# Kernel optimization log

Measured on AMD Instinct MI355X. Metric: run time of the kernel, lower is better.

## Reference

```python
import jax, jax.numpy as jnp
import numpy as np

K = 3      # deformable kernel size
PAD = 1    # padding for all 3x3 convs


def conv2d(x, w, b):
    y = jax.lax.conv_general_dilated(x, w, (1, 1), ((PAD, PAD), (PAD, PAD)),
                                     dimension_numbers=('NCHW', 'OIHW', 'NCHW'))
    return y + b[None, :, None, None]


def ln_channels(x, w, b, eps=1e-5):
    # Restormer 'WithBias' LayerNorm: normalize over channel dim of NCHW
    mu = jnp.mean(x, axis=1, keepdims=True)
    var = jnp.mean((x - mu) ** 2, axis=1, keepdims=True)
    return (x - mu) / jnp.sqrt(var + eps) * w[None, :, None, None] + b[None, :, None, None]


def deform_conv(x, offset, mask, weight, bias):
    # x: [B,Cin,H,W], offset: [B,2*K*K,H,W] (dy,dx interleaved), mask: [B,K*K,H,W]
    B, Cin, H, W = x.shape
    Kk = K * K
    off = offset.reshape(B, Kk, 2, H, W)
    dy, dx = off[:, :, 0], off[:, :, 1]                     # [B,Kk,H,W]
    ky, kx = jnp.meshgrid(jnp.arange(K), jnp.arange(K), indexing='ij')
    ky = (ky.reshape(-1) - PAD).astype(x.dtype)             # [Kk]
    kx = (kx.reshape(-1) - PAD).astype(x.dtype)
    py = jnp.arange(H, dtype=x.dtype)[None, None, :, None] + ky[None, :, None, None] + dy
    px = jnp.arange(W, dtype=x.dtype)[None, None, None, :] + kx[None, :, None, None] + dx
    y0 = jnp.floor(py); x0 = jnp.floor(px)
    wy1 = py - y0; wx1 = px - x0
    xf = x.reshape(B, Cin, H * W)

    def corner(yc, xc, wgt):
        valid = (yc >= 0) & (yc <= H - 1) & (xc >= 0) & (xc <= W - 1)
        yi = jnp.clip(yc, 0, H - 1).astype(jnp.int32)
        xi = jnp.clip(xc, 0, W - 1).astype(jnp.int32)
        idx = (yi * W + xi).reshape(B, -1)                  # [B, Kk*H*W]
        v = jax.vmap(lambda xb, ib: xb[:, ib])(xf, idx)     # [B, Cin, Kk*H*W]
        v = v.reshape(B, Cin, Kk, H, W)
        return v * (wgt * valid.astype(x.dtype))[:, None]

    sampled = (corner(y0, x0, (1 - wy1) * (1 - wx1))
               + corner(y0, x0 + 1, (1 - wy1) * wx1)
               + corner(y0 + 1, x0, wy1 * (1 - wx1))
               + corner(y0 + 1, x0 + 1, wy1 * wx1))         # [B,Cin,Kk,H,W]
    sampled = sampled * mask[:, None]                        # modulated (DCNv2)
    wk = weight.reshape(weight.shape[0], Cin, Kk)            # [Cout,Cin,Kk]
    out = jnp.einsum('bckhw,ock->bohw', sampled, wk)
    return out + bias[None, :, None, None]


def setup_inputs() -> dict:
    key = jax.random.key(0)
    ks = jax.random.split(key, 12)
    B, Ce, Cf, H, W = 4, 32, 64, 128, 128
    Cin, Kk = Ce + Cf, K * K
    d = {
        'f_evt_rec': jax.random.normal(ks[0], (B, Ce, H, W), jnp.float32),
        'f_efnet':   jax.random.normal(ks[1], (B, Cf, H, W), jnp.float32),
        'ln_evt_w': jnp.ones((Ce,), jnp.float32), 'ln_evt_b': jnp.zeros((Ce,), jnp.float32),
        'ln_ef_w':  jnp.ones((Cf,), jnp.float32), 'ln_ef_b':  jnp.zeros((Cf,), jnp.float32),
        'ln_al_w':  jnp.ones((Cf,), jnp.float32), 'ln_al_b':  jnp.zeros((Cf,), jnp.float32),
        'off_w': jax.random.normal(ks[2], (2 * Kk, Cin, K, K), jnp.float32) * 0.01,
        'off_b': jnp.zeros((2 * Kk,), jnp.float32),
        'mod_w': jax.random.normal(ks[3], (Kk, Cin, K, K), jnp.float32) * 0.01,
        'mod_b': jnp.zeros((Kk,), jnp.float32),
        'reg_w': jax.random.normal(ks[4], (Cf, Cin, K, K), jnp.float32) * 0.05,
        'reg_b': jnp.zeros((Cf,), jnp.float32),
        'stage_idx': 0,
    }
    return d


def reference(f_evt_rec, f_efnet, ln_evt_w, ln_evt_b, ln_ef_w, ln_ef_b,
              ln_al_w, ln_al_b, off_w, off_b, mod_w, mod_b, reg_w, reg_b, stage_idx):
    e = ln_channels(f_evt_rec, ln_evt_w, ln_evt_b)
    fe = ln_channels(f_efnet, ln_ef_w, ln_ef_b)
    ox = jnp.concatenate([e, fe], axis=1)                    # [B,96,H,W]
    offset = conv2d(ox, off_w, off_b)
    mask = 2.0 * jax.nn.sigmoid(conv2d(ox, mod_w, mod_b))
    al = deform_conv(ox, offset, mask, reg_w, reg_b)         # [B,64,H,W]
    al = jnp.where(al >= 0, al, 0.2 * al)                    # LeakyReLU(0.2)
    al = ln_channels(al, ln_al_w, ln_al_b)
    return al
```

## Files before the change

kernel.cpp:

```cpp
#include <hip/hip_runtime.h>
#include <hip/hip_bf16.h>

#define BATCH 4
#define HH 128
#define WW 128
#define CE 32
#define CF 64
#define CIN 96
#define KK 9
#define COUT 64

typedef __bf16 bf16x8 __attribute__((ext_vector_type(8)));
typedef float f32x4 __attribute__((ext_vector_type(4)));
#define MFMA16(a, b, c) __builtin_amdgcn_mfma_f32_16x16x32_bf16(a, b, c, 0, 0, 0)
typedef union { uint4 u; bf16x8 v; } U8;

#define OX_BYTES   (BATCH * HH * WW * CIN * 2)
#define WCT_OFFB   OX_BYTES
#define WCT_BYTES  (32 * 864 * 2)
#define WKT_OFFB   (WCT_OFFB + WCT_BYTES)

__global__ __launch_bounds__(256) void ln_concat_prep(
    const float* __restrict__ evt, const float* __restrict__ efn,
    const float* __restrict__ w_e, const float* __restrict__ b_e,
    const float* __restrict__ w_f, const float* __restrict__ b_f,
    const float* __restrict__ off_w, const float* __restrict__ mod_w,
    const float* __restrict__ reg_w,
    __hip_bfloat16* __restrict__ ox,
    __hip_bfloat16* __restrict__ wcombT,
    __hip_bfloat16* __restrict__ wkT) {
  __shared__ float vals[64 * 97];
  __shared__ float part[4 * 64 * 4];
  __shared__ float stat[64 * 4];

  {
    int e = blockIdx.x * 256 + threadIdx.x;
    const int TOT1 = 32 * 864, TOT2 = 64 * 864;
    if (e < TOT1) {
      int oc = e / 864, k = e % 864;
      int tap = k / 96, c = k % 96;
      float v = 0.f;
      if (oc < 18)      v = off_w[(oc * CIN + c) * KK + tap];
      else if (oc < 27) v = mod_w[((oc - 18) * CIN + c) * KK + tap];
      wcombT[e] = __float2bfloat16(v);
    } else if (e < TOT1 + TOT2) {
      int e2 = e - TOT1;
      int oc = e2 / 864, k = e2 % 864;
      int tap = k / 96, c = k % 96;
      wkT[e2] = __float2bfloat16(reg_w[(oc * CIN + c) * KK + tap]);
    }
  }

  int bid = blockIdx.x;
  int wg = (bid & 7) * 128 + (bid >> 3);
  int p0 = wg * 64;
  int b = p0 >> 14, y = (p0 >> 7) & 127, x0 = p0 & 127;
  int t = threadIdx.x, px = t & 63, g = t >> 6;

  float sE = 0.f, sE2 = 0.f, sF = 0.f, sF2 = 0.f;
  const float* pe = evt + (((size_t)b * CE) << 14) + (y << 7) + x0 + px;
#pragma unroll
  for (int j = 0; j < 8; ++j) {
    int c = g * 8 + j;
    float v = pe[(size_t)c << 14];
    vals[px * 97 + c] = v; sE += v; sE2 += v * v;
  }
  const float* pf = efn + (((size_t)b * CF) << 14) + (y << 7) + x0 + px;
#pragma unroll
  for (int j = 0; j < 16; ++j) {
    int c = g * 16 + j;
    float v = pf[(size_t)c << 14];
    vals[px * 97 + CE + c] = v; sF += v; sF2 += v * v;
  }
  {
    float4 p4 = {sE, sE2, sF, sF2};
    *(float4*)&part[(g * 64 + px) * 4] = p4;
  }
  __syncthreads();
  if (g == 0) {
    float aE = 0.f, aE2 = 0.f, aF = 0.f, aF2 = 0.f;
#pragma unroll
    for (int gg = 0; gg < 4; ++gg) {
      float4 p4 = *(const float4*)&part[(gg * 64 + px) * 4];
      aE += p4.x; aE2 += p4.y; aF += p4.z; aF2 += p4.w;
    }
    float muE = aE * (1.f / CE);
    float vE = aE2 * (1.f / CE) - muE * muE;
    float muF = aF * (1.f / CF);
    float vF = aF2 * (1.f / CF) - muF * muF;
    float4 s4 = {muE, rsqrtf(vE + 1e-5f), muF, rsqrtf(vF + 1e-5f)};
    *(float4*)&stat[px * 4] = s4;
  }
  __syncthreads();
  uint* orow = (uint*)(ox + (size_t)p0 * CIN);
#pragma unroll
  for (int i = 0; i < 12; ++i) {
    int e = i * 256 + t;
    int xx = e / 48, c = (e % 48) * 2;
    float v0 = vals[xx * 97 + c], v1 = vals[xx * 97 + c + 1];
    float mu, rs, lw0, lb0, lw1, lb1;
    if (c < CE) {
      mu = stat[xx * 4 + 0]; rs = stat[xx * 4 + 1];
      lw0 = w_e[c]; lb0 = b_e[c]; lw1 = w_e[c + 1]; lb1 = b_e[c + 1];
    } else {
      mu = stat[xx * 4 + 2]; rs = stat[xx * 4 + 3];
      lw0 = w_f[c - CE]; lb0 = b_f[c - CE]; lw1 = w_f[c + 1 - CE]; lb1 = b_f[c + 1 - CE];
    }
    float o0 = (v0 - mu) * rs * lw0 + lb0;
    float o1 = (v1 - mu) * rs * lw1 + lb1;
    __hip_bfloat16 h0 = __float2bfloat16(o0), h1 = __float2bfloat16(o1);
    orow[e] = ((uint)*(unsigned short*)&h1 << 16) | (uint)*(unsigned short*)&h0;
  }
}

__device__ __forceinline__ uint blend1(uint u0, uint u1, uint u2, uint u3,
                                       float w0, float w1, float w2, float w3) {
  float lo = w0 * __uint_as_float(u0 << 16) + w1 * __uint_as_float(u1 << 16)
           + w2 * __uint_as_float(u2 << 16) + w3 * __uint_as_float(u3 << 16);
  float hi = w0 * __uint_as_float(u0 & 0xffff0000u) + w1 * __uint_as_float(u1 & 0xffff0000u)
           + w2 * __uint_as_float(u2 & 0xffff0000u) + w3 * __uint_as_float(u3 & 0xffff0000u);
  __hip_bfloat16 bl = __float2bfloat16(lo), bh = __float2bfloat16(hi);
  return ((uint)*(unsigned short*)&bh << 16) | (uint)*(unsigned short*)&bl;
}

__global__ __launch_bounds__(256, 4) void conv_deform_fused(
    const __hip_bfloat16* __restrict__ ox,
    const __hip_bfloat16* __restrict__ wcombT,
    const __hip_bfloat16* __restrict__ wkT,
    const float* __restrict__ off_b, const float* __restrict__ mod_b,
    const float* __restrict__ reg_b,
    const float* __restrict__ lnw, const float* __restrict__ lnb,
    float* __restrict__ out) {
  __shared__ float offm[64 * 28];
  __shared__ float outl[64 * 65];

  int bid = blockIdx.x;
  int wg = (bid & 7) * 128 + (bid >> 3);
  int p0 = wg * 64;
  int b = p0 >> 14, y = (p0 >> 7) & 127, x0 = p0 & 127;
  const __hip_bfloat16* oxb = ox + (((size_t)b) << 14) * CIN;

  int t = threadIdx.x, lane = t & 63, wv = t >> 6;
  int lr = lane & 15, lg = lane >> 4;
  int pxw = (wv << 4) + lr;

  f32x4 cc0 = {0.f,0.f,0.f,0.f}, cc1 = {0.f,0.f,0.f,0.f};
  {
    const __hip_bfloat16* br0 = wcombT + (size_t)lr * 864 + lg * 8;
    const __hip_bfloat16* br1 = wcombT + (size_t)(16 + lr) * 864 + lg * 8;
    for (int tap = 0; tap < 9; ++tap) {
      int yy = y + tap / 3 - 1;
      int xx = x0 + pxw + tap % 3 - 1;
      bool valid = ((unsigned)yy < 128u) && ((unsigned)xx < 128u);
      int cy = min(max(yy, 0), 127), cx = min(max(xx, 0), 127);
      const __hip_bfloat16* arow = oxb + (size_t)((cy << 7) + cx) * CIN + lg * 8;
#pragma unroll
      for (int ks = 0; ks < 3; ++ks) {
        U8 a, w0, w1;
        a.u = *(const uint4*)(arow + ks * 32);
        if (!valid) { a.u.x = 0; a.u.y = 0; a.u.z = 0; a.u.w = 0; }
        w0.u = *(const uint4*)(br0 + tap * 96 + ks * 32);
        w1.u = *(const uint4*)(br1 + tap * 96 + ks * 32);
        cc0 = MFMA16(a.v, w0.v, cc0);
        cc1 = MFMA16(a.v, w1.v, cc1);
      }
    }
  }
#pragma unroll
  for (int nt = 0; nt < 2; ++nt) {
    int oc = nt * 16 + lr;
    if (oc < 27) {
      float bia = (oc < 18) ? off_b[oc] : mod_b[oc - 18];
      f32x4 a = nt ? cc1 : cc0;
#pragma unroll
      for (int r = 0; r < 4; ++r) {
        int pxc = (wv << 4) + (lg << 2) + r;
        float v = a[r] + bia;
        if (oc >= 18) v = 2.f / (1.f + __expf(-v));
        offm[pxc * 28 + oc] = v;
      }
    }
  }

  const float* om = offm + pxw * 28;
  const __hip_bfloat16* gb = oxb + lg * 8;
  f32x4 ac0 = {0.f,0.f,0.f,0.f}, ac1 = {0.f,0.f,0.f,0.f};
  f32x4 ac2 = {0.f,0.f,0.f,0.f}, ac3 = {0.f,0.f,0.f,0.f};

  uint4 qa0,qa1,qa2,qa3, qb0,qb1,qb2,qb3, qc0,qc1,qc2,qc3;
  float pw0, pw1, pw2, pw3;

#define ISSUE(T)                                                             \
  {                                                                          \
    float dyv = om[2 * (T)], dxv = om[2 * (T) + 1], mk = om[18 + (T)];       \
    float psy = (float)(y + (T) / 3 - 1) + dyv;                              \
    float psx = (float)(x0 + pxw + (T) % 3 - 1) + dxv;                       \
    float fy = floorf(psy), fx = floorf(psx);                                \
    float wy1 = psy - fy, wx1 = psx - fx;                                    \
    float wy0 = 1.f - wy1, wx0 = 1.f - wx1;                                  \
    int iy0 = (int)fy, ix0 = (int)fx, iy1 = iy0 + 1, ix1 = ix0 + 1;          \
    float vy0 = ((unsigned)iy0 < 128u) ? 1.f : 0.f;                          \
    float vy1 = ((unsigned)iy1 < 128u) ? 1.f : 0.f;                          \
    float vx0 = ((unsigned)ix0 < 128u) ? 1.f : 0.f;                          \
    float vx1 = ((unsigned)ix1 < 128u) ? 1.f : 0.f;                          \
    int cy0 = min(max(iy0, 0), 127), cy1 = min(max(iy1, 0), 127);            \
    int cx0 = min(max(ix0, 0), 127), cx1 = min(max(ix1, 0), 127);            \
    int i00 = ((cy0 << 7) + cx0) * CIN, i01 = ((cy0 << 7) + cx1) * CIN;      \
    int i10 = ((cy1 << 7) + cx0) * CIN, i11 = ((cy1 << 7) + cx1) * CIN;      \
    pw0 = wy0 * wx0 * vy0 * vx0 * mk; pw1 = wy0 * wx1 * vy0 * vx1 * mk;      \
    pw2 = wy1 * wx0 * vy1 * vx0 * mk; pw3 = wy1 * wx1 * vy1 * vx1 * mk;      \
    qa0 = *(const uint4*)(gb + i00);      qa1 = *(const uint4*)(gb + i01);   \
    qa2 = *(const uint4*)(gb + i10);      qa3 = *(const uint4*)(gb + i11);   \
    qb0 = *(const uint4*)(gb + i00 + 32); qb1 = *(const uint4*)(gb + i01 + 32);\
    qb2 = *(const uint4*)(gb + i10 + 32); qb3 = *(const uint4*)(gb + i11 + 32);\
    qc0 = *(const uint4*)(gb + i00 + 64); qc1 = *(const uint4*)(gb + i01 + 64);\
    qc2 = *(const uint4*)(gb + i10 + 64); qc3 = *(const uint4*)(gb + i11 + 64);\
  }

  ISSUE(0);
  for (int tap = 0; tap < 9; ++tap) {
    U8 fa0, fa1, fa2;
    fa0.u.x = blend1(qa0.x, qa1.x, qa2.x, qa3.x, pw0, pw1, pw2, pw3);
    fa0.u.y = blend1(qa0.y, qa1.y, qa2.y, qa3.y, pw0, pw1, pw2, pw3);
    fa0.u.z = blend1(qa0.z, qa1.z, qa2.z, qa3.z, pw0, pw1, pw2, pw3);
    fa0.u.w = blend1(qa0.w, qa1.w, qa2.w, qa3.w, pw0, pw1, pw2, pw3);
    fa1.u.x = blend1(qb0.x, qb1.x, qb2.x, qb3.x, pw0, pw1, pw2, pw3);
    fa1.u.y = blend1(qb0.y, qb1.y, qb2.y, qb3.y, pw0, pw1, pw2, pw3);
    fa1.u.z = blend1(qb0.z, qb1.z, qb2.z, qb3.z, pw0, pw1, pw2, pw3);
    fa1.u.w = blend1(qb0.w, qb1.w, qb2.w, qb3.w, pw0, pw1, pw2, pw3);
    fa2.u.x = blend1(qc0.x, qc1.x, qc2.x, qc3.x, pw0, pw1, pw2, pw3);
    fa2.u.y = blend1(qc0.y, qc1.y, qc2.y, qc3.y, pw0, pw1, pw2, pw3);
    fa2.u.z = blend1(qc0.z, qc1.z, qc2.z, qc3.z, pw0, pw1, pw2, pw3);
    fa2.u.w = blend1(qc0.w, qc1.w, qc2.w, qc3.w, pw0, pw1, pw2, pw3);
    if (tap < 8) {
      int tn = tap + 1;
      ISSUE(tn);
    }
    const __hip_bfloat16* wr = wkT + (size_t)lr * 864 + tap * 96 + lg * 8;
    U8 b0, b1, b2;
#define MSTEP(ACC, ROWOFF)                                                   \
    b0.u = *(const uint4*)(wr + (ROWOFF) * 864);                             \
    b1.u = *(const uint4*)(wr + (ROWOFF) * 864 + 32);                        \
    b2.u = *(const uint4*)(wr + (ROWOFF) * 864 + 64);                        \
    ACC = MFMA16(fa0.v, b0.v, ACC);                                          \
    ACC = MFMA16(fa1.v, b1.v, ACC);                                          \
    ACC = MFMA16(fa2.v, b2.v, ACC);
    MSTEP(ac0, 0)
    MSTEP(ac1, 16)
    MSTEP(ac2, 32)
    MSTEP(ac3, 48)
#undef MSTEP
  }
#undef ISSUE

#pragma unroll
  for (int nt = 0; nt < 4; ++nt) {
    int oc = nt * 16 + lr;
    float bia = reg_b[oc];
    f32x4 a = (nt == 0) ? ac0 : (nt == 1) ? ac1 : (nt == 2) ? ac2 : ac3;
#pragma unroll
    for (int r = 0; r < 4; ++r) {
      int pxc = (wv << 4) + (lg << 2) + r;
      float v = a[r] + bia;
      v = (v >= 0.f) ? v : 0.2f * v;
      outl[pxc * 65 + oc] = v;
    }
  }
  {
    int px2 = (wv << 4) + (lane >> 2);
    int part = lane & 3;
    float s = 0.f, s2 = 0.f;
#pragma unroll
    for (int j = 0; j < 16; ++j) {
      float v = outl[px2 * 65 + part * 16 + j];
      s += v; s2 += v * v;
    }
    s += __shfl_xor(s, 1); s2 += __shfl_xor(s2, 1);
    s += __shfl_xor(s, 2); s2 += __shfl_xor(s2, 2);
    float mu = s * (1.f / 64.f);
    float var = s2 * (1.f / 64.f) - mu * mu;
    float rs = rsqrtf(var + 1e-5f);
    size_t ob = (size_t)b * COUT * 16384 + (size_t)y * 128 + x0 + px2;
#pragma unroll
    for (int j = 0; j < 16; ++j) {
      int oc = part * 16 + j;
      float v = outl[px2 * 65 + oc];
      out[ob + (size_t)oc * 16384] = (v - mu) * rs * lnw[oc] + lnb[oc];
    }
  }
}

extern "C" void kernel_launch(void* const* d_in, const int* in_sizes, int n_in,
                              void* d_out, int out_size, void* d_ws, size_t ws_size,
                              hipStream_t stream) {
  const float* evt      = (const float*)d_in[0];
  const float* efn      = (const float*)d_in[1];
  const float* ln_evt_w = (const float*)d_in[2];
  const float* ln_evt_b = (const float*)d_in[3];
  const float* ln_ef_w  = (const float*)d_in[4];
  const float* ln_ef_b  = (const float*)d_in[5];
  const float* ln_al_w  = (const float*)d_in[6];
  const float* ln_al_b  = (const float*)d_in[7];
  const float* off_w    = (const float*)d_in[8];
  const float* off_b    = (const float*)d_in[9];
  const float* mod_w    = (const float*)d_in[10];
  const float* mod_b    = (const float*)d_in[11];
  const float* reg_w    = (const float*)d_in[12];
  const float* reg_b    = (const float*)d_in[13];
  float* out = (float*)d_out;

  char* wsb = (char*)d_ws;
  __hip_bfloat16* oxb    = (__hip_bfloat16*)wsb;
  __hip_bfloat16* wcombT = (__hip_bfloat16*)(wsb + WCT_OFFB);
  __hip_bfloat16* wkT    = (__hip_bfloat16*)(wsb + WKT_OFFB);

  ln_concat_prep<<<BATCH * HH * WW / 64, 256, 0, stream>>>(
      evt, efn, ln_evt_w, ln_evt_b, ln_ef_w, ln_ef_b,
      off_w, mod_w, reg_w, oxb, wcombT, wkT);
  conv_deform_fused<<<BATCH * HH * WW / 64, 256, 0, stream>>>(
      oxb, wcombT, wkT, off_b, mod_b, reg_b, ln_al_w, ln_al_b, out);
}
```

Measured before the change: 188.7 us.

## Shrink fused deform kernel to one wave per block with fine-grained gather pipeline

Changes the fused conv+deform kernel from 256-thread blocks covering 64 pixels to 64-thread single-wave blocks covering 16 pixels, launching four times as many blocks. The weights are re-laid out per (tap, k-slice) as contiguous 32-wide chunks so each MFMA weight fetch reads a compact block. The deform loop is restructured to 27 fully unrolled k-steps that double-buffer one 32-channel gather at a time rather than three per tap. The intent is lower register pressure, higher occupancy and finer latency hiding of the bilinear gathers. The trade-off is more blocks and more redundant weight loads per pixel.

Measured after the change: 186.3 us. No clear change (-1.3%).

```diff
diff --git a/kernel.cpp b/kernel.cpp
--- a/kernel.cpp
+++ b/kernel.cpp
@@ -7,7 +7,6 @@
 #define CE 32
 #define CF 64
 #define CIN 96
-#define KK 9
 #define COUT 64
 
 typedef __bf16 bf16x8 __attribute__((ext_vector_type(8)));
@@ -17,8 +16,9 @@
 
 #define OX_BYTES   (BATCH * HH * WW * CIN * 2)
 #define WCT_OFFB   OX_BYTES
-#define WCT_BYTES  (32 * 864 * 2)
+#define WCT_BYTES  (27 * 32 * 32 * 2)
 #define WKT_OFFB   (WCT_OFFB + WCT_BYTES)
+
 
 __global__ __launch_bounds__(256) void ln_concat_prep(
     const float* __restrict__ evt, const float* __restrict__ efn,
@@ -27,27 +27,30 @@
     const float* __restrict__ off_w, const float* __restrict__ mod_w,
     const float* __restrict__ reg_w,
     __hip_bfloat16* __restrict__ ox,
-    __hip_bfloat16* __restrict__ wcombT,
-    __hip_bfloat16* __restrict__ wkT) {
+    __hip_bfloat16* __restrict__ wcombT2,
+    __hip_bfloat16* __restrict__ wkT2) {
   __shared__ float vals[64 * 97];
   __shared__ float part[4 * 64 * 4];
   __shared__ float stat[64 * 4];
 
   {
     int e = blockIdx.x * 256 + threadIdx.x;
-    const int TOT1 = 32 * 864, TOT2 = 64 * 864;
+    const int TOT1 = 27 * 32 * 32;
+    const int TOT2 = 27 * 64 * 32;
     if (e < TOT1) {
-      int oc = e / 864, k = e % 864;
-      int tap = k / 96, c = k % 96;
+      int r = e & 31, g = e >> 5;
+      int oc = g & 31, tks = g >> 5;
+      int tap = tks / 3, ks = tks % 3, c = ks * 32 + r;
       float v = 0.f;
-      if (oc < 18)      v = off_w[(oc * CIN + c) * KK + tap];
-      else if (oc < 27) v = mod_w[((oc - 18) * CIN + c) * KK + tap];
-      wcombT[e] = __float2bfloat16(v);
+      if (oc < 18)      v = off_w[(oc * CIN + c) * 9 + tap];
+      else if (oc < 27) v = mod_w[((oc - 18) * CIN + c) * 9 + tap];
+      wcombT2[e] = __float2bfloat16(v);
     } else if (e < TOT1 + TOT2) {
       int e2 = e - TOT1;
-      int oc = e2 / 864, k = e2 % 864;
-      int tap = k / 96, c = k % 96;
-      wkT[e2] = __float2bfloat16(reg_w[(oc * CIN + c) * KK + tap]);
+      int r = e2 & 31, g = e2 >> 5;
+      int oc = g & 63, tks = g >> 6;
+      int tap = tks / 3, ks = tks % 3, c = ks * 32 + r;
+      wkT2[e2] = __float2bfloat16(reg_w[(oc * CIN + c) * 9 + tap]);
     }
   }
 
@@ -123,47 +126,43 @@
   return ((uint)*(unsigned short*)&bh << 16) | (uint)*(unsigned short*)&bl;
 }
 
-__global__ __launch_bounds__(256, 4) void conv_deform_fused(
+__global__ __launch_bounds__(64) void conv_deform_fused(
     const __hip_bfloat16* __restrict__ ox,
-    const __hip_bfloat16* __restrict__ wcombT,
-    const __hip_bfloat16* __restrict__ wkT,
+    const __hip_bfloat16* __restrict__ wct2,
+    const __hip_bfloat16* __restrict__ wkt2,
     const float* __restrict__ off_b, const float* __restrict__ mod_b,
     const float* __restrict__ reg_b,
     const float* __restrict__ lnw, const float* __restrict__ lnb,
     float* __restrict__ out) {
-  __shared__ float offm[64 * 28];
-  __shared__ float outl[64 * 65];
+  __shared__ float offm[16 * 28];
+  __shared__ float outl[16 * 65];
 
   int bid = blockIdx.x;
-  int wg = (bid & 7) * 128 + (bid >> 3);
-  int p0 = wg * 64;
+  int wg = (bid & 7) * 512 + (bid >> 3);
+  int p0 = wg * 16;
   int b = p0 >> 14, y = (p0 >> 7) & 127, x0 = p0 & 127;
   const __hip_bfloat16* oxb = ox + (((size_t)b) << 14) * CIN;
 
-  int t = threadIdx.x, lane = t & 63, wv = t >> 6;
-  int lr = lane & 15, lg = lane >> 4;
-  int pxw = (wv << 4) + lr;
+  int lane = threadIdx.x, lr = lane & 15, lg = lane >> 4;
 
   f32x4 cc0 = {0.f,0.f,0.f,0.f}, cc1 = {0.f,0.f,0.f,0.f};
-  {
-    const __hip_bfloat16* br0 = wcombT + (size_t)lr * 864 + lg * 8;
-    const __hip_bfloat16* br1 = wcombT + (size_t)(16 + lr) * 864 + lg * 8;
-    for (int tap = 0; tap < 9; ++tap) {
-      int yy = y + tap / 3 - 1;
-      int xx = x0 + pxw + tap % 3 - 1;
-      bool valid = ((unsigned)yy < 128u) && ((unsigned)xx < 128u);
-      int cy = min(max(yy, 0), 127), cx = min(max(xx, 0), 127);
-      const __hip_bfloat16* arow = oxb + (size_t)((cy << 7) + cx) * CIN + lg * 8;
-#pragma unroll
-      for (int ks = 0; ks < 3; ++ks) {
-        U8 a, w0, w1;
-        a.u = *(const uint4*)(arow + ks * 32);
-        if (!valid) { a.u.x = 0; a.u.y = 0; a.u.z = 0; a.u.w = 0; }
-        w0.u = *(const uint4*)(br0 + tap * 96 + ks * 32);
-        w1.u = *(const uint4*)(br1 + tap * 96 + ks * 32);
-        cc0 = MFMA16(a.v, w0.v, cc0);
-        cc1 = MFMA16(a.v, w1.v, cc1);
-      }
+#pragma unroll
+  for (int tap = 0; tap < 9; ++tap) {
+    int yy = y + tap / 3 - 1;
+    int xx = x0 + lr + tap % 3 - 1;
+    bool valid = ((unsigned)yy < 128u) && ((unsigned)xx < 128u);
+    int cy = min(max(yy, 0), 127), cx = min(max(xx, 0), 127);
+    const __hip_bfloat16* arow = oxb + (size_t)((cy << 7) + cx) * CIN + lg * 8;
+#pragma unroll
+    for (int ks = 0; ks < 3; ++ks) {
+      U8 a, w0, w1;
+      a.u = *(const uint4*)(arow + ks * 32);
+      if (!valid) { a.u.x = 0; a.u.y = 0; a.u.z = 0; a.u.w = 0; }
+      const __hip_bfloat16* wb = wct2 + (size_t)((tap * 3 + ks) * 32) * 32 + lg * 8;
+      w0.u = *(const uint4*)(wb + lr * 32);
+      w1.u = *(const uint4*)(wb + (16 + lr) * 32);
+      cc0 = MFMA16(a.v, w0.v, cc0);
+      cc1 = MFMA16(a.v, w1.v, cc1);
     }
   }
 #pragma unroll
@@ -174,84 +173,90 @@
       f32x4 a = nt ? cc1 : cc0;
 #pragma unroll
       for (int r = 0; r < 4; ++r) {
-        int pxc = (wv << 4) + (lg << 2) + r;
         float v = a[r] + bia;
         if (oc >= 18) v = 2.f / (1.f + __expf(-v));
-        offm[pxc * 28 + oc] = v;
+        offm[(lg * 4 + r) * 28 + oc] = v;
       }
     }
   }
-
-  const float* om = offm + pxw * 28;
-  const __hip_bfloat16* gb = oxb + lg * 8;
+  __syncthreads();
+
+  const float* om = offm + lr * 28;
   f32x4 ac0 = {0.f,0.f,0.f,0.f}, ac1 = {0.f,0.f,0.f,0.f};
   f32x4 ac2 = {0.f,0.f,0.f,0.f}, ac3 = {0.f,0.f,0.f,0.f};
 
-  uint4 qa0,qa1,qa2,qa3, qb0,qb1,qb2,qb3, qc0,qc1,qc2,qc3;
-  float pw0, pw1, pw2, pw3;
-
-#define ISSUE(T)                                                             \
-  {                                                                          \
-    float dyv = om[2 * (T)], dxv = om[2 * (T) + 1], mk = om[18 + (T)];       \
-    float psy = (float)(y + (T) / 3 - 1) + dyv;                              \
-    float psx = (float)(x0 + pxw + (T) % 3 - 1) + dxv;                       \
-    float fy = floorf(psy), fx = floorf(psx);                                \
-    float wy1 = psy - fy, wx1 = psx - fx;                                    \
-    float wy0 = 1.f - wy1, wx0 = 1.f - wx1;                                  \
-    int iy0 = (int)fy, ix0 = (int)fx, iy1 = iy0 + 1, ix1 = ix0 + 1;          \
-    float vy0 = ((unsigned)iy0 < 128u) ? 1.f : 0.f;                          \
-    float vy1 = ((unsigned)iy1 < 128u) ? 1.f : 0.f;                          \
-    float vx0 = ((unsigned)ix0 < 128u) ? 1.f : 0.f;                          \
-    float vx1 = ((unsigned)ix1 < 128u) ? 1.f : 0.f;                          \
-    int cy0 = min(max(iy0, 0), 127), cy1 = min(max(iy1, 0), 127);            \
-    int cx0 = min(max(ix0, 0), 127), cx1 = min(max(ix1, 0), 127);            \
-    int i00 = ((cy0 << 7) + cx0) * CIN, i01 = ((cy0 << 7) + cx1) * CIN;      \
-    int i10 = ((cy1 << 7) + cx0) * CIN, i11 = ((cy1 << 7) + cx1) * CIN;      \
-    pw0 = wy0 * wx0 * vy0 * vx0 * mk; pw1 = wy0 * wx1 * vy0 * vx1 * mk;      \
-    pw2 = wy1 * wx0 * vy1 * vx0 * mk; pw3 = wy1 * wx1 * vy1 * vx1 * mk;      \
-    qa0 = *(const uint4*)(gb + i00);      qa1 = *(const uint4*)(gb + i01);   \
-    qa2 = *(const uint4*)(gb + i10);      qa3 = *(const uint4*)(gb + i11);   \
-    qb0 = *(const uint4*)(gb + i00 + 32); qb1 = *(const uint4*)(gb + i01 + 32);\
-    qb2 = *(const uint4*)(gb + i10 + 32); qb3 = *(const uint4*)(gb + i11 + 32);\
-    qc0 = *(const uint4*)(gb + i00 + 64); qc1 = *(const uint4*)(gb + i01 + 64);\
-    qc2 = *(const uint4*)(gb + i10 + 64); qc3 = *(const uint4*)(gb + i11 + 64);\
-  }
-
-  ISSUE(0);
-  for (int tap = 0; tap < 9; ++tap) {
-    U8 fa0, fa1, fa2;
-    fa0.u.x = blend1(qa0.x, qa1.x, qa2.x, qa3.x, pw0, pw1, pw2, pw3);
-    fa0.u.y = blend1(qa0.y, qa1.y, qa2.y, qa3.y, pw0, pw1, pw2, pw3);
-    fa0.u.z = blend1(qa0.z, qa1.z, qa2.z, qa3.z, pw0, pw1, pw2, pw3);
-    fa0.u.w = blend1(qa0.w, qa1.w, qa2.w, qa3.w, pw0, pw1, pw2, pw3);
-    fa1.u.x = blend1(qb0.x, qb1.x, qb2.x, qb3.x, pw0, pw1, pw2, pw3);
-    fa1.u.y = blend1(qb0.y, qb1.y, qb2.y, qb3.y, pw0, pw1, pw2, pw3);
-    fa1.u.z = blend1(qb0.z, qb1.z, qb2.z, qb3.z, pw0, pw1, pw2, pw3);
-    fa1.u.w = blend1(qb0.w, qb1.w, qb2.w, qb3.w, pw0, pw1, pw2, pw3);
-    fa2.u.x = blend1(qc0.x, qc1.x, qc2.x, qc3.x, pw0, pw1, pw2, pw3);
-    fa2.u.y = blend1(qc0.y, qc1.y, qc2.y, qc3.y, pw0, pw1, pw2, pw3);
-    fa2.u.z = blend1(qc0.z, qc1.z, qc2.z, qc3.z, pw0, pw1, pw2, pw3);
-    fa2.u.w = blend1(qc0.w, qc1.w, qc2.w, qc3.w, pw0, pw1, pw2, pw3);
-    if (tap < 8) {
-      int tn = tap + 1;
-      ISSUE(tn);
-    }
-    const __hip_bfloat16* wr = wkT + (size_t)lr * 864 + tap * 96 + lg * 8;
-    U8 b0, b1, b2;
-#define MSTEP(ACC, ROWOFF)                                                   \
-    b0.u = *(const uint4*)(wr + (ROWOFF) * 864);                             \
-    b1.u = *(const uint4*)(wr + (ROWOFF) * 864 + 32);                        \
-    b2.u = *(const uint4*)(wr + (ROWOFF) * 864 + 64);                        \
-    ACC = MFMA16(fa0.v, b0.v, ACC);                                          \
-    ACC = MFMA16(fa1.v, b1.v, ACC);                                          \
-    ACC = MFMA16(fa2.v, b2.v, ACC);
-    MSTEP(ac0, 0)
-    MSTEP(ac1, 16)
-    MSTEP(ac2, 32)
-    MSTEP(ac3, 48)
-#undef MSTEP
-  }
-#undef ISSUE
+  uint4 q[2][4];
+  int   idx[2][4];
+  float pwv[2][4];
+
+#define PARAMS(T, S)                                                          \
+  {                                                                           \
+    float dyv = om[2 * (T)], dxv = om[2 * (T) + 1], mk = om[18 + (T)];        \
+    float psy = (float)(y + (T) / 3 - 1) + dyv;                               \
+    float psx = (float)(x0 + lr + (T) % 3 - 1) + dxv;                         \
+    float fy = floorf(psy), fx = floorf(psx);                                 \
+    float wy1 = psy - fy, wx1 = psx - fx;                                     \
+    float wy0 = 1.f - wy1, wx0 = 1.f - wx1;                                   \
+    int iy0 = (int)fy, ix0 = (int)fx, iy1 = iy0 + 1, ix1 = ix0 + 1;           \
+    float vy0 = ((unsigned)iy0 < 128u) ? 1.f : 0.f;                           \
+    float vy1 = ((unsigned)iy1 < 128u) ? 1.f : 0.f;                           \
+    float vx0 = ((unsigned)ix0 < 128u) ? 1.f : 0.f;                           \
+    float vx1 = ((unsigned)ix1 < 128u) ? 1.f : 0.f;                           \
+    int cy0 = min(max(iy0, 0), 127), cy1 = min(max(iy1, 0), 127);             \
+    int cx0 = min(max(ix0, 0), 127), cx1 = min(max(ix1, 0), 127);             \
+    idx[S][0] = ((cy0 << 7) + cx0) * CIN;                                     \
+    idx[S][1] = ((cy0 << 7) + cx1) * CIN;                                     \
+    idx[S][2] = ((cy1 << 7) + cx0) * CIN;                                     \
+    idx[S][3] = ((cy1 << 7) + cx1) * CIN;                                     \
+    pwv[S][0] = wy0 * wx0 * vy0 * vx0 * mk;                                   \
+    pwv[S][1] = wy0 * wx1 * vy0 * vx1 * mk;                                   \
+    pwv[S][2] = wy1 * wx0 * vy1 * vx0 * mk;                                   \
+    pwv[S][3] = wy1 * wx1 * vy1 * vx1 * mk;                                   \
+  }
+
+#define GATHER(QS, PS, KOFF)                                                  \
+  {                                                                           \
+    q[QS][0] = *(const uint4*)(oxb + idx[PS][0] + (KOFF));                    \
+    q[QS][1] = *(const uint4*)(oxb + idx[PS][1] + (KOFF));                    \
+    q[QS][2] = *(const uint4*)(oxb + idx[PS][2] + (KOFF));                    \
+    q[QS][3] = *(const uint4*)(oxb + idx[PS][3] + (KOFF));                    \
+  }
+
+  PARAMS(0, 0);
+  GATHER(0, 0, lg * 8);
+
+#pragma unroll
+  for (int cc = 0; cc < 27; ++cc) {
+    const int tap = cc / 3, ks = cc % 3;
+    const int cur = cc & 1, tp = tap & 1;
+    const __hip_bfloat16* wb = wkt2 + (size_t)((tap * 3 + ks) * 64) * 32 + lg * 8;
+    U8 b0, b1, b2, b3;
+    b0.u = *(const uint4*)(wb + lr * 32);
+    b1.u = *(const uint4*)(wb + (16 + lr) * 32);
+    b2.u = *(const uint4*)(wb + (32 + lr) * 32);
+    b3.u = *(const uint4*)(wb + (48 + lr) * 32);
+    U8 fa;
+    fa.u.x = blend1(q[cur][0].x, q[cur][1].x, q[cur][2].x, q[cur][3].x,
+                    pwv[tp][0], pwv[tp][1], pwv[tp][2], pwv[tp][3]);
+    fa.u.y = blend1(q[cur][0].y, q[cur][1].y, q[cur][2].y, q[cur][3].y,
+                    pwv[tp][0], pwv[tp][1], pwv[tp][2], pwv[tp][3]);
+    fa.u.z = blend1(q[cur][0].z, q[cur][1].z, q[cur][2].z, q[cur][3].z,
+                    pwv[tp][0], pwv[tp][1], pwv[tp][2], pwv[tp][3]);
+    fa.u.w = blend1(q[cur][0].w, q[cur][1].w, q[cur][2].w, q[cur][3].w,
+                    pwv[tp][0], pwv[tp][1], pwv[tp][2], pwv[tp][3]);
+    if (cc < 26) {
+      const int nc = cc + 1, ntap = nc / 3, nks = nc % 3;
+      const int nxt = nc & 1, ntp = ntap & 1;
+      if (nks == 0) PARAMS(ntap, ntp);
+      GATHER(nxt, ntp, nks * 32 + lg * 8);
+    }
+    ac0 = MFMA16(fa.v, b0.v, ac0);
+    ac1 = MFMA16(fa.v, b1.v, ac1);
+    ac2 = MFMA16(fa.v, b2.v, ac2);
+    ac3 = MFMA16(fa.v, b3.v, ac3);
+  }
+#undef PARAMS
+#undef GATHER
 
 #pragma unroll
   for (int nt = 0; nt < 4; ++nt) {
@@ -260,15 +265,14 @@
     f32x4 a = (nt == 0) ? ac0 : (nt == 1) ? ac1 : (nt == 2) ? ac2 : ac3;
 #pragma unroll
     for (int r = 0; r < 4; ++r) {
-      int pxc = (wv << 4) + (lg << 2) + r;
       float v = a[r] + bia;
       v = (v >= 0.f) ? v : 0.2f * v;
-      outl[pxc * 65 + oc] = v;
-    }
-  }
+      outl[(lg * 4 + r) * 65 + oc] = v;
+    }
+  }
+  __syncthreads();
   {
-    int px2 = (wv << 4) + (lane >> 2);
-    int part = lane & 3;
+    int px2 = lane >> 2, part = lane & 3;
     float s = 0.f, s2 = 0.f;
 #pragma unroll
     for (int j = 0; j < 16; ++j) {
@@ -311,12 +315,12 @@
 
   char* wsb = (char*)d_ws;
   __hip_bfloat16* oxb    = (__hip_bfloat16*)wsb;
-  __hip_bfloat16* wcombT = (__hip_bfloat16*)(wsb + WCT_OFFB);
-  __hip_bfloat16* wkT    = (__hip_bfloat16*)(wsb + WKT_OFFB);
+  __hip_bfloat16* wct2   = (__hip_bfloat16*)(wsb + WCT_OFFB);
+  __hip_bfloat16* wkt2   = (__hip_bfloat16*)(wsb + WKT_OFFB);
 
   ln_concat_prep<<<BATCH * HH * WW / 64, 256, 0, stream>>>(
       evt, efn, ln_evt_w, ln_evt_b, ln_ef_w, ln_ef_b,
-      off_w, mod_w, reg_w, oxb, wcombT, wkT);
-  conv_deform_fused<<<BATCH * HH * WW / 64, 256, 0, stream>>>(
-      oxb, wcombT, wkT, off_b, mod_b, reg_b, ln_al_w, ln_al_b, out);
+      off_w, mod_w, reg_w, oxb, wct2, wkt2);
+  conv_deform_fused<<<BATCH * HH * WW / 16, 64, 0, stream>>>(
+      oxb, wct2, wkt2, off_b, mod_b, reg_b, ln_al_w, ln_al_b, out);
 }
```
